# Kernel optimization log

Measured on AMD Instinct MI355X. Metric: run time of the kernel, lower is better.

The kernel has to match this reference:

```python
import jax, jax.numpy as jnp
import numpy as np

EMB = 128   # emb_dim
NT = 4      # n_ntype
ET = 38     # n_etype
H = 4       # head_count
DH = EMB // H


def _bn(x, g, b):
    # BatchNorm1d in training mode: batch stats, biased variance, eps=1e-5
    m = x.mean(0)
    v = ((x - m) ** 2).mean(0)
    return (x - m) * jax.lax.rsqrt(v + 1e-5) * g + b


def setup_inputs() -> dict:
    key = jax.random.key(0)
    ks = jax.random.split(key, 32)
    N, E, d = 20000, 320000, EMB
    fe = ET + 1 + 2 * NT  # 47 = edge one-hot + head/tail one-hots
    s = 0.05
    inp = {
        "x": jax.random.normal(ks[0], (N, d), jnp.float32),
        "node_feature_extra": jax.random.normal(ks[1], (N, d), jnp.float32),
        "edge_index": jax.random.randint(ks[2], (2, E), 0, N),
        "edge_type": jax.random.randint(ks[3], (E,), 0, ET),
        "node_type": jax.random.randint(ks[4], (N,), 0, NT),
        # edge_encoder: Linear(47,d) + BN(d) + ReLU + Linear(d,d)
        "We1": jax.random.normal(ks[5], (fe, d), jnp.float32) * s,
        "be1": jax.random.normal(ks[6], (d,), jnp.float32) * s,
        "ge": 1.0 + jax.random.normal(ks[7], (d,), jnp.float32) * 0.1,
        "bbe": jax.random.normal(ks[8], (d,), jnp.float32) * 0.1,
        "We2": jax.random.normal(ks[9], (d, d), jnp.float32) * s,
        "be2": jax.random.normal(ks[10], (d,), jnp.float32) * s,
        # attention linears
        "Wk": jax.random.normal(ks[11], (3 * d, d), jnp.float32) * s,
        "bk": jax.random.normal(ks[12], (d,), jnp.float32) * s,
        "Wm": jax.random.normal(ks[13], (3 * d, d), jnp.float32) * s,
        "bm": jax.random.normal(ks[14], (d,), jnp.float32) * s,
        "Wq": jax.random.normal(ks[15], (2 * d, d), jnp.float32) * s,
        "bq": jax.random.normal(ks[16], (d,), jnp.float32) * s,
        # output mlp: Linear(d,d) + BN(d) + ReLU + Linear(d,d)
        "Wo1": jax.random.normal(ks[17], (d, d), jnp.float32) * s,
        "bo1": jax.random.normal(ks[18], (d,), jnp.float32) * s,
        "go": 1.0 + jax.random.normal(ks[19], (d,), jnp.float32) * 0.1,
        "bbo": jax.random.normal(ks[20], (d,), jnp.float32) * 0.1,
        "Wo2": jax.random.normal(ks[21], (d, d), jnp.float32) * s,
        "bo2": jax.random.normal(ks[22], (d,), jnp.float32) * s,
    }
    return inp


def reference(x, node_feature_extra, edge_index, edge_type, node_type,
              We1, be1, ge, bbe, We2, be2, Wk, bk, Wm, bm, Wq, bq,
              Wo1, bo1, go, bbo, Wo2, bo2):
    N, d = x.shape
    src0, dst0 = edge_index[0], edge_index[1]

    # edge features: one-hot edge type (+ self-loop type ET) || head/tail node-type one-hots
    ev = jax.nn.one_hot(edge_type, ET + 1, dtype=x.dtype)                  # [E, 39]
    self_ev = jnp.zeros((N, ET + 1), x.dtype).at[:, ET].set(1.0)           # [N, 39]
    nvec = jax.nn.one_hot(node_type, NT, dtype=x.dtype)                    # [N, 4]
    ht = jnp.concatenate([nvec[src0], nvec[dst0]], 1)                      # [E, 8]
    sht = jnp.concatenate([nvec, nvec], 1)                                 # [N, 8]
    feats = jnp.concatenate([jnp.concatenate([ev, ht], 1),
                             jnp.concatenate([self_ev, sht], 1)], 0)       # [E+N, 47]

    # edge_encoder MLP (BN over all E+N rows, training-mode stats)
    edge_attr = jax.nn.relu(_bn(feats @ We1 + be1, ge, bbe)) @ We2 + be2   # [E+N, d]

    loop = jnp.arange(N)
    src = jnp.concatenate([src0, loop])   # message source / softmax groups
    dst = jnp.concatenate([dst0, loop])   # aggregation target (x_i)

    X2 = jnp.concatenate([x, node_feature_extra], 1)                       # [N, 2d]
    xi = X2[dst]                                                           # [Et, 2d]
    xj = X2[src]                                                           # [Et, 2d]

    # split matmuls == Linear(concat([x, edge_attr]))
    k = (xi @ Wk[:2 * d] + edge_attr @ Wk[2 * d:] + bk).reshape(-1, H, DH)
    m = (xj @ Wm[:2 * d] + edge_attr @ Wm[2 * d:] + bm).reshape(-1, H, DH)
    q = ((xj @ Wq + bq) / np.sqrt(DH).astype(np.float32)).reshape(-1, H, DH)
    scores = (q * k).sum(-1)                                               # [Et, H]

    # scatter softmax over source node index
    smax = jax.lax.stop_gradient(jax.ops.segment_max(scores, src, num_segments=N))
    ex = jnp.exp(scores - smax[src])
    denom = jax.ops.segment_sum(ex, src, num_segments=N)
    alpha = ex / (denom[src] + 1e-16)

    # degree rescaling
    cnt = jax.ops.segment_sum(jnp.ones((src.shape[0],), x.dtype), src, num_segments=N)[src]
    alpha = alpha * cnt[:, None]

    out_msg = (m * alpha[:, :, None]).reshape(-1, d)
    aggr = jax.ops.segment_sum(out_msg, dst, num_segments=N)               # [N, d]

    # output MLP
    return jax.nn.relu(_bn(aggr @ Wo1 + bo1, go, bbo)) @ Wo2 + bo2
```

## Files before the change

kernel.cpp:

```cpp
#include <hip/hip_runtime.h>
#include <math.h>


#define ET_N 38
#define NCOMBO 624
#define NB_CNT 64
#define HALF_MAX 10240

__global__ __launch_bounds__(256) void count_kernel(
    const int* __restrict__ ei, const int* __restrict__ et,
    const int* __restrict__ nt, int* __restrict__ ce,
    unsigned* __restrict__ ph, unsigned* __restrict__ ps,
    unsigned* __restrict__ pd, int E, int Et, int N) {
  __shared__ unsigned lcnt[HALF_MAX];
  __shared__ unsigned lhist[NCOMBO];
  const int b = blockIdx.x;
  const int half = blockIdx.y & 1, which = blockIdx.y >> 1;
  const int H = (N + 1) >> 1;
  const int lo = half * H, hi = min(N, lo + H);
  const int span = hi - lo;
  const bool do_ce = (which == 0 && half == 0);
  for (int i = threadIdx.x; i < span; i += 256) lcnt[i] = 0;
  if (do_ce)
    for (int i = threadIdx.x; i < NCOMBO; i += 256) lhist[i] = 0;
  __syncthreads();
  const int chunk = (Et + NB_CNT - 1) / NB_CNT;
  const int e0 = b * chunk, e1 = min(Et, e0 + chunk);
  for (int e = e0 + threadIdx.x; e < e1; e += 256) {
    if (which == 0) {
      int s = (e < E) ? ei[e] : e - E;
      if (s >= lo && s < hi) atomicAdd(&lcnt[s - lo], 1u);
      if (do_ce) {
        int d = (e < E) ? ei[E + e] : e - E;
        int t = (e < E) ? et[e] : ET_N;
        int c = t * 16 + nt[s] * 4 + nt[d];
        ce[e] = c;
        atomicAdd(&lhist[c], 1u);
      }
    } else {
      int d = (e < E) ? ei[E + e] : e - E;
      if (d >= lo && d < hi) atomicAdd(&lcnt[d - lo], 1u);
    }
  }
  __syncthreads();
  unsigned* out = (which == 0) ? ps : pd;
  for (int i = threadIdx.x; i < span; i += 256)
    out[(size_t)b * N + lo + i] = lcnt[i];
  if (do_ce)
    for (int i = threadIdx.x; i < NCOMBO; i += 256)
      ph[(size_t)b * NCOMBO + i] = lhist[i];
}

__global__ __launch_bounds__(128) void histred_kernel(
    const unsigned* __restrict__ ph, int* __restrict__ hist) {
  int c = blockIdx.x * 128 + threadIdx.x;
  if (c >= NCOMBO) return;
  unsigned s = 0;
  for (int b = 0; b < NB_CNT; b++) s += ph[(size_t)b * NCOMBO + c];
  hist[c] = (int)s;
}

__global__ __launch_bounds__(256) void cntred_kernel(
    const unsigned* __restrict__ ps, const unsigned* __restrict__ pd,
    int* __restrict__ scnt, int* __restrict__ dcnt, int N) {
  int i = blockIdx.x * 256 + threadIdx.x;
  if (i >= 2 * N) return;
  const unsigned* src = (i < N) ? ps : pd;
  int n = (i < N) ? i : i - N;
  unsigned s = 0;
  for (int b = 0; b < NB_CNT; b++) s += src[(size_t)b * N + n];
  if (i < N) scnt[n] = (int)s;
  else       dcnt[n] = (int)s;
}

__global__ __launch_bounds__(1024) void scan_kernel(
    const int* __restrict__ dcnt, int* __restrict__ doff, int n) {
  __shared__ int s[1024];
  int tid = threadIdx.x;
  int ch = (n + 1023) >> 10;
  int base = tid * ch;
  int sum = 0;
  for (int i = 0; i < ch; i++) { int idx = base + i; if (idx < n) sum += dcnt[idx]; }
  s[tid] = sum; __syncthreads();
  for (int off = 1; off < 1024; off <<= 1) {
    int v = (tid >= off) ? s[tid - off] : 0;
    __syncthreads();
    s[tid] += v;
    __syncthreads();
  }
  int run = (tid > 0) ? s[tid - 1] : 0;
  for (int i = 0; i < ch; i++) {
    int idx = base + i;
    if (idx < n) { doff[idx] = run; run += dcnt[idx]; }
  }
  if (tid == 1023) doff[n] = s[1023];
}

__global__ __launch_bounds__(256) void bucket_kernel(
    const int* __restrict__ ei, const int* __restrict__ ce,
    const int* __restrict__ doff, int* __restrict__ dctr,
    int* __restrict__ ebuck, unsigned* __restrict__ sb, int E, int Et) {
  int e = blockIdx.x * 256 + threadIdx.x;
  if (e >= Et) return;
  int s, d;
  if (e < E) { s = ei[e]; d = ei[E + e]; }
  else       { s = d = e - E; }
  int c = ce[e];
  int pos = atomicAdd(&dctr[(size_t)d * 16], 1);
  int idx = doff[d] + pos;
  ebuck[idx] = e;
  sb[idx] = (unsigned)s | ((unsigned)c << 15);
}

__global__ __launch_bounds__(128) void bnstats1_kernel(
    const int* __restrict__ hist, const float* __restrict__ We1,
    const float* __restrict__ be1, const float* __restrict__ ge,
    const float* __restrict__ bbe, float* __restrict__ a1,
    float* __restrict__ b1, float invR) {
  int j = threadIdx.x;
  float s1 = 0.f, s2 = 0.f;
  for (int c = 0; c < NCOMBO; c++) {
    int w = hist[c];
    if (!w) continue;
    int t = c >> 4, a = (c >> 2) & 3, b = c & 3;
    float v = We1[t * 128 + j] + We1[(39 + a) * 128 + j] + We1[(43 + b) * 128 + j] + be1[j];
    float wf = (float)w;
    s1 += wf * v;
    s2 += wf * v * v;
  }
  float mean = s1 * invR;
  float var  = s2 * invR - mean * mean;
  float av = ge[j] * rsqrtf(var + 1e-5f);
  a1[j] = av;
  b1[j] = bbe[j] - mean * av;
}

__global__ __launch_bounds__(256) void htab_kernel(
    const float* __restrict__ We1, const float* __restrict__ be1,
    const float* __restrict__ a1, const float* __restrict__ b1,
    float* __restrict__ H) {
  int i = blockIdx.x * 256 + threadIdx.x;
  if (i >= NCOMBO * 128) return;
  int c = i >> 7, j = i & 127;
  int t = c >> 4, a = (c >> 2) & 3, b = c & 3;
  float v = We1[t * 128 + j] + We1[(39 + a) * 128 + j] + We1[(43 + b) * 128 + j] + be1[j];
  H[i] = fmaxf(0.f, v * a1[j] + b1[j]);
}

template <class ALoad>
static __device__ __forceinline__ void gemm_body(
    ALoad aload, const float* __restrict__ B, const float* __restrict__ bias,
    float* __restrict__ C, int M, int K, float scale, int row0) {
  __shared__ float As[16][68];
  __shared__ float Bs[16][128];
  const int tid = threadIdx.x;
  const int ty = tid >> 4, tx = tid & 15;
  float acc[4][8];
#pragma unroll
  for (int i = 0; i < 4; i++)
#pragma unroll
    for (int j = 0; j < 8; j++) acc[i][j] = 0.f;

  const int ar = tid >> 2;
  const int ak = (tid & 3) << 2;
  const int bk = tid >> 5;
  const int bc = (tid & 31) << 2;

  for (int k0 = 0; k0 < K; k0 += 16) {
    float4 av = make_float4(0.f, 0.f, 0.f, 0.f);
    int grow = row0 + ar;
    if (grow < M) av = aload(grow, k0 + ak);
    As[ak + 0][ar] = av.x;
    As[ak + 1][ar] = av.y;
    As[ak + 2][ar] = av.z;
    As[ak + 3][ar] = av.w;
    float4 b0 = *(const float4*)(B + (size_t)(k0 + bk) * 128 + bc);
    float4 b1 = *(const float4*)(B + (size_t)(k0 + bk + 8) * 128 + bc);
    *(float4*)&Bs[bk][bc] = b0;
    *(float4*)&Bs[bk + 8][bc] = b1;
    __syncthreads();
#pragma unroll
    for (int kk = 0; kk < 16; kk++) {
      float4 a4 = *(const float4*)&As[kk][ty << 2];
      float4 p0 = *(const float4*)&Bs[kk][tx << 2];
      float4 p1 = *(const float4*)&Bs[kk][64 + (tx << 2)];
      float a_[4] = {a4.x, a4.y, a4.z, a4.w};
      float b_[8] = {p0.x, p0.y, p0.z, p0.w, p1.x, p1.y, p1.z, p1.w};
#pragma unroll
      for (int i = 0; i < 4; i++)
#pragma unroll
        for (int j = 0; j < 8; j++) acc[i][j] = fmaf(a_[i], b_[j], acc[i][j]);
    }
    __syncthreads();
  }
#pragma unroll
  for (int i = 0; i < 4; i++) {
    int gr = row0 + (ty << 2) + i;
    if (gr >= M) continue;
    float out[8];
#pragma unroll
    for (int j = 0; j < 8; j++) {
      int col = (j < 4) ? (tx << 2) + j : 64 + (tx << 2) + (j - 4);
      float bv = bias ? bias[col] : 0.f;
      out[j] = (acc[i][j] + bv) * scale;
    }
    float4* cp0 = (float4*)(C + (size_t)gr * 128 + (tx << 2));
    float4* cp1 = (float4*)(C + (size_t)gr * 128 + 64 + (tx << 2));
    cp0[0] = make_float4(out[0], out[1], out[2], out[3]);
    cp1[0] = make_float4(out[4], out[5], out[6], out[7]);
  }
}

__global__ __launch_bounds__(256) void tab2_kernel(
    const float* __restrict__ Ttab,
    const float* __restrict__ WkE, const float* __restrict__ bk,
    const float* __restrict__ WmE, const float* __restrict__ bm,
    float* __restrict__ Tk, float* __restrict__ Tm) {
  const int row0 = blockIdx.x * 64;
  const float* B    = blockIdx.y ? WmE : WkE;
  const float* bias = blockIdx.y ? bm : bk;
  float*       C    = blockIdx.y ? Tm : Tk;
  auto aload = [&](int grow, int k) -> float4 {
    return *(const float4*)(Ttab + (size_t)grow * 128 + k);
  };
  gemm_body(aload, B, bias, C, NCOMBO, 128, 1.0f, row0);
}

__global__ __launch_bounds__(256) void node3_kernel(
    const float* __restrict__ x, const float* __restrict__ nfe,
    const float* __restrict__ Wk, const float* __restrict__ Wm,
    const float* __restrict__ Wq, const float* __restrict__ bq,
    float* __restrict__ K1n, float* __restrict__ M1n, float* __restrict__ Qn,
    int N) {
  const int row0 = blockIdx.x * 64;
  const float* B;
  const float* bias;
  float* C;
  float scale;
  if (blockIdx.y == 0)      { B = Wk; bias = nullptr; C = K1n; scale = 1.0f; }
  else if (blockIdx.y == 1) { B = Wm; bias = nullptr; C = M1n; scale = 1.0f; }
  else                      { B = Wq; bias = bq;      C = Qn;  scale = 0.17677669529663687f; }
  auto aload = [&](int grow, int k) -> float4 {
    const float* src = (k < 128) ? x : nfe;
    return *(const float4*)(src + (size_t)grow * 128 + (k & 127));
  };
  gemm_body(aload, B, bias, C, N, 256, scale, row0);
}

template <bool TRANS>
__global__ __launch_bounds__(256) void gemm_plain(
    const float* __restrict__ A, const float* __restrict__ B,
    const float* __restrict__ bias, const float* __restrict__ ta,
    const float* __restrict__ tb, float* __restrict__ C,
    int M, int K, float scale) {
  const int row0 = blockIdx.x * 64;
  auto aload = [&](int grow, int k) -> float4 {
    float4 v = *(const float4*)(A + (size_t)grow * K + k);
    if (TRANS) {
      v.x = fmaxf(0.f, fmaf(v.x, ta[k + 0], tb[k + 0]));
      v.y = fmaxf(0.f, fmaf(v.y, ta[k + 1], tb[k + 1]));
      v.z = fmaxf(0.f, fmaf(v.z, ta[k + 2], tb[k + 2]));
      v.w = fmaxf(0.f, fmaf(v.w, ta[k + 3], tb[k + 3]));
    }
    return v;
  };
  gemm_body(aload, B, bias, C, M, K, scale, row0);
}

__global__ __launch_bounds__(256) void score_kernel(
    const int* __restrict__ ei, const int* __restrict__ ce,
    const float* __restrict__ Qn, const float* __restrict__ K1n,
    const float* __restrict__ Tk, float* __restrict__ ex,
    float* __restrict__ denomp, int E, int Et) {
  int g0 = (blockIdx.x * 8 + (threadIdx.x >> 5)) * 2;
  int lane = threadIdx.x & 31;
  if (g0 >= Et) return;
  int g1 = g0 + 1;
  bool v1 = g1 < Et;

  int s0, d0;
  if (g0 < E) { s0 = ei[g0]; d0 = ei[E + g0]; }
  else        { s0 = d0 = g0 - E; }
  int c0 = ce[g0];
  int s1 = 0, d1 = 0, c1 = 0;
  if (v1) {
    if (g1 < E) { s1 = ei[g1]; d1 = ei[E + g1]; }
    else        { s1 = d1 = g1 - E; }
    c1 = ce[g1];
  }

  float4 q0 = ((const float4*)(Qn  + (size_t)s0 * 128))[lane];
  float4 k0 = ((const float4*)(K1n + (size_t)d0 * 128))[lane];
  float4 t0 = ((const float4*)(Tk  + (size_t)c0 * 128))[lane];
  float4 q1 = ((const float4*)(Qn  + (size_t)s1 * 128))[lane];
  float4 k1 = ((const float4*)(K1n + (size_t)d1 * 128))[lane];
  float4 t1 = ((const float4*)(Tk  + (size_t)c1 * 128))[lane];

  float p0 = q0.x * (k0.x + t0.x) + q0.y * (k0.y + t0.y) +
             q0.z * (k0.z + t0.z) + q0.w * (k0.w + t0.w);
  float p1 = q1.x * (k1.x + t1.x) + q1.y * (k1.y + t1.y) +
             q1.z * (k1.z + t1.z) + q1.w * (k1.w + t1.w);
  p0 += __shfl_xor(p0, 4); p1 += __shfl_xor(p1, 4);
  p0 += __shfl_xor(p0, 2); p1 += __shfl_xor(p1, 2);
  p0 += __shfl_xor(p0, 1); p1 += __shfl_xor(p1, 1);

  if ((lane & 7) == 0) {
    int h = lane >> 3;
    float e0 = expf(p0);
    ex[(size_t)g0 * 4 + h] = e0;
    atomicAdd(&denomp[(size_t)s0 * 16 + h], e0);
    if (v1) {
      float e1 = expf(p1);
      ex[(size_t)g1 * 4 + h] = e1;
      atomicAdd(&denomp[(size_t)s1 * 16 + h], e1);
    }
  }
}

__global__ __launch_bounds__(256) void rden_kernel(
    const int* __restrict__ scnt, float* __restrict__ denomp, int N) {
  int i = blockIdx.x * 256 + threadIdx.x;
  if (i >= N * 4) return;
  int n = i >> 2, h = i & 3;
  float v = denomp[(size_t)n * 16 + h];
  denomp[(size_t)n * 16 + h] = (float)scnt[n] / (v + 1e-16f);
}

__global__ __launch_bounds__(256) void alphab_kernel(
    const int* __restrict__ ebuck, const unsigned* __restrict__ sb,
    const float* __restrict__ ex, const float* __restrict__ denomp,
    float* __restrict__ ab, int Et) {
  int idx = blockIdx.x * 256 + threadIdx.x;
  if (idx >= Et) return;
  int e = ebuck[idx];
  int s = sb[idx] & 0x7FFF;
  float4 exv = ((const float4*)ex)[e];
  float4 dn  = *(const float4*)&denomp[(size_t)s * 16];
  ((float4*)ab)[idx] = make_float4(exv.x * dn.x, exv.y * dn.y,
                                   exv.z * dn.z, exv.w * dn.w);
}

__global__ __launch_bounds__(256) void aggr_kernel(
    const unsigned* __restrict__ sb, const float* __restrict__ ab,
    const int* __restrict__ doff, const float* __restrict__ M1n,
    const float* __restrict__ Tm, float* __restrict__ aggr) {
  __shared__ float sacc[128];
  int n = blockIdx.x;
  int j = threadIdx.x & 127;
  int half = threadIdx.x >> 7;
  int h = j >> 5;
  float acc = 0.f;
  int i0 = doff[n], i1 = doff[n + 1];
  for (int base = i0 + half * 2; base < i1; base += 4) {
    int kA = base, kB = base + 1;
    unsigned pA = sb[kA];
    int sA = pA & 0x7FFF, cA = pA >> 15;
    float alA = ab[(size_t)kA * 4 + h];
    float mA = M1n[(size_t)sA * 128 + j] + Tm[(size_t)cA * 128 + j];
    bool vB = kB < i1;
    unsigned pB = vB ? sb[kB] : 0u;
    int sB = pB & 0x7FFF, cB = pB >> 15;
    float alB = vB ? ab[(size_t)kB * 4 + h] : 0.f;
    float mB = vB ? (M1n[(size_t)sB * 128 + j] + Tm[(size_t)cB * 128 + j]) : 0.f;
    acc += mA * alA;
    acc += mB * alB;
  }
  if (half == 1) sacc[j] = acc;
  __syncthreads();
  if (half == 0) aggr[(size_t)n * 128 + j] = acc + sacc[j];
}

__global__ __launch_bounds__(256) void colsum_kernel(
    const float* __restrict__ z, float* __restrict__ s1,
    float* __restrict__ s2, int M) {
  __shared__ float l1[256], l2[256];
  int j = threadIdx.x & 127;
  int half = threadIdx.x >> 7;
  float a = 0.f, b = 0.f;
  for (int r = blockIdx.x * 2 + half; r < M; r += gridDim.x * 2) {
    float v = z[(size_t)r * 128 + j];
    a += v;
    b += v * v;
  }
  l1[threadIdx.x] = a;
  l2[threadIdx.x] = b;
  __syncthreads();
  if (half == 0) {
    a = l1[j] + l1[j + 128];
    b = l2[j] + l2[j + 128];
    atomicAdd(&s1[j], a);
    atomicAdd(&s2[j], b);
  }
}

__global__ __launch_bounds__(128) void bnparam_kernel(
    const float* __restrict__ s1, const float* __restrict__ s2,
    const float* __restrict__ g, const float* __restrict__ bb,
    float* __restrict__ ta, float* __restrict__ tb, float invM) {
  int j = threadIdx.x;
  float mean = s1[j] * invM;
  float var = s2[j] * invM - mean * mean;
  float a = g[j] * rsqrtf(var + 1e-5f);
  ta[j] = a;
  tb[j] = bb[j] - mean * a;
}

extern "C" void kernel_launch(void* const* d_in, const int* in_sizes, int n_in,
                              void* d_out, int out_size, void* d_ws, size_t ws_size,
                              hipStream_t stream) {
  const float* x   = (const float*)d_in[0];
  const float* nfe = (const float*)d_in[1];
  const int*   ei  = (const int*)d_in[2];
  const int*   et  = (const int*)d_in[3];
  const int*   nt  = (const int*)d_in[4];
  const float* We1 = (const float*)d_in[5];
  const float* be1 = (const float*)d_in[6];
  const float* ge  = (const float*)d_in[7];
  const float* bbe = (const float*)d_in[8];
  const float* We2 = (const float*)d_in[9];
  const float* be2 = (const float*)d_in[10];
  const float* Wk  = (const float*)d_in[11];
  const float* bkb = (const float*)d_in[12];
  const float* Wm  = (const float*)d_in[13];
  const float* bmb = (const float*)d_in[14];
  const float* Wq  = (const float*)d_in[15];
  const float* bqb = (const float*)d_in[16];
  const float* Wo1 = (const float*)d_in[17];
  const float* bo1 = (const float*)d_in[18];
  const float* go  = (const float*)d_in[19];
  const float* bbo = (const float*)d_in[20];
  const float* Wo2 = (const float*)d_in[21];
  const float* bo2 = (const float*)d_in[22];

  const int N  = in_sizes[0] / 128;
  const int E  = in_sizes[3];
  const int Et = E + N;

  char* p = (char*)d_ws;
  auto alloc = [&](size_t bytes) -> char* {
    char* r = p;
    p += (bytes + 255) & ~(size_t)255;
    return r;
  };
  char* zero_base = p;
  int*   dctr  = (int*)alloc((size_t)N * 16 * 4);
  float* denomp= (float*)alloc((size_t)N * 16 * 4);
  float* cs1   = (float*)alloc(128 * 4);
  float* cs2   = (float*)alloc(128 * 4);
  size_t zero_bytes = (size_t)(p - zero_base);
  int*      ce   = (int*)alloc((size_t)Et * 4);
  int*      ebuck= (int*)alloc((size_t)Et * 4);
  unsigned* sb   = (unsigned*)alloc((size_t)Et * 4);
  int*      doff = (int*)alloc((size_t)(N + 1) * 4);
  int*      hist = (int*)alloc(NCOMBO * 4);
  int*      scnt = (int*)alloc((size_t)N * 4);
  int*      dcnt = (int*)alloc((size_t)N * 4);
  unsigned* ps   = (unsigned*)alloc((size_t)NB_CNT * N * 4);
  unsigned* pd   = (unsigned*)alloc((size_t)NB_CNT * N * 4);
  unsigned* ph   = (unsigned*)alloc((size_t)NB_CNT * NCOMBO * 4);
  float* a1    = (float*)alloc(128 * 4);
  float* b1    = (float*)alloc(128 * 4);
  float* a2    = (float*)alloc(128 * 4);
  float* b2    = (float*)alloc(128 * 4);
  float* Htab  = (float*)alloc((size_t)NCOMBO * 128 * 4);
  float* Ttab  = (float*)alloc((size_t)NCOMBO * 128 * 4);
  float* Tk    = (float*)alloc((size_t)NCOMBO * 128 * 4);
  float* Tm    = (float*)alloc((size_t)NCOMBO * 128 * 4);
  float* K1n   = (float*)alloc((size_t)N * 128 * 4);
  float* M1n   = (float*)alloc((size_t)N * 128 * 4);
  float* Qn    = (float*)alloc((size_t)N * 128 * 4);
  float* exbuf = (float*)alloc((size_t)Et * 4 * 4);
  float* ab    = (float*)alloc((size_t)Et * 4 * 4);
  float* aggr  = (float*)alloc((size_t)N * 128 * 4);
  float* z     = (float*)alloc((size_t)N * 128 * 4);
  (void)ws_size;

  hipMemsetAsync(zero_base, 0, zero_bytes, stream);

  count_kernel<<<dim3(NB_CNT, 4), 256, 0, stream>>>(ei, et, nt, ce, ph, ps, pd, E, Et, N);
  histred_kernel<<<(NCOMBO + 127) / 128, 128, 0, stream>>>(ph, hist);
  cntred_kernel<<<(2 * N + 255) / 256, 256, 0, stream>>>(ps, pd, scnt, dcnt, N);
  scan_kernel<<<1, 1024, 0, stream>>>(dcnt, doff, N);
  bucket_kernel<<<(Et + 255) / 256, 256, 0, stream>>>(ei, ce, doff, dctr, ebuck, sb, E, Et);
  bnstats1_kernel<<<1, 128, 0, stream>>>(hist, We1, be1, ge, bbe, a1, b1, 1.0f / (float)Et);
  htab_kernel<<<(NCOMBO * 128 + 255) / 256, 256, 0, stream>>>(We1, be1, a1, b1, Htab);
  gemm_plain<false><<<(NCOMBO + 63) / 64, 256, 0, stream>>>(Htab, We2, be2, nullptr, nullptr, Ttab, NCOMBO, 128, 1.0f);
  tab2_kernel<<<dim3((NCOMBO + 63) / 64, 2), 256, 0, stream>>>(Ttab, Wk + 256 * 128, bkb, Wm + 256 * 128, bmb, Tk, Tm);
  int gm = (N + 63) / 64;
  node3_kernel<<<dim3(gm, 3), 256, 0, stream>>>(x, nfe, Wk, Wm, Wq, bqb, K1n, M1n, Qn, N);
  score_kernel<<<(Et + 15) / 16, 256, 0, stream>>>(ei, ce, Qn, K1n, Tk, exbuf, denomp, E, Et);
  rden_kernel<<<(N * 4 + 255) / 256, 256, 0, stream>>>(scnt, denomp, N);
  alphab_kernel<<<(Et + 255) / 256, 256, 0, stream>>>(ebuck, sb, exbuf, denomp, ab, Et);
  aggr_kernel<<<N, 256, 0, stream>>>(sb, ab, doff, M1n, Tm, aggr);
  gemm_plain<false><<<gm, 256, 0, stream>>>(aggr, Wo1, bo1, nullptr, nullptr, z, N, 128, 1.0f);
  colsum_kernel<<<256, 256, 0, stream>>>(z, cs1, cs2, N);
  bnparam_kernel<<<1, 128, 0, stream>>>(cs1, cs2, go, bbo, a2, b2, 1.0f / (float)N);
  gemm_plain<true><<<gm, 256, 0, stream>>>(z, Wo2, bo2, a2, b2, (float*)d_out, N, 128, 1.0f);
}
```

Baseline: 527.4 us.

## Scatter exp scores into dst-bucket order and fold alpha into aggregation

The bucket kernel now records each edge's bucket position, so the score kernel writes exp values directly in destination-sorted order. This removes the alphab pass and its intermediate buffer; the aggregation kernel multiplies by the per-source reciprocal denominator inline and is unrolled four deep. The edge-encoder BN statistics are also split into a precomputed value table, a 16-block partial reduction and a separate parameter kernel. The BN+ReLU is applied inside the GEMM's A-load instead of through a separate htab pass. The cost is scattered 4-byte writes in the score kernel and an extra gather of denomp per edge in aggregation.

```diff
diff --git a/kernel.cpp b/kernel.cpp
--- a/kernel.cpp
+++ b/kernel.cpp
@@ -5,6 +5,7 @@
 #define ET_N 38
 #define NCOMBO 624
 #define NB_CNT 64
+#define NB_ST 16
 #define HALF_MAX 10240
 
 __global__ __launch_bounds__(256) void count_kernel(
@@ -99,7 +100,7 @@
 __global__ __launch_bounds__(256) void bucket_kernel(
     const int* __restrict__ ei, const int* __restrict__ ce,
     const int* __restrict__ doff, int* __restrict__ dctr,
-    int* __restrict__ ebuck, unsigned* __restrict__ sb, int E, int Et) {
+    unsigned* __restrict__ sb, int* __restrict__ ibuck, int E, int Et) {
   int e = blockIdx.x * 256 + threadIdx.x;
   if (e >= Et) return;
   int s, d;
@@ -108,43 +109,45 @@
   int c = ce[e];
   int pos = atomicAdd(&dctr[(size_t)d * 16], 1);
   int idx = doff[d] + pos;
-  ebuck[idx] = e;
   sb[idx] = (unsigned)s | ((unsigned)c << 15);
-}
-
-__global__ __launch_bounds__(128) void bnstats1_kernel(
-    const int* __restrict__ hist, const float* __restrict__ We1,
-    const float* __restrict__ be1, const float* __restrict__ ge,
-    const float* __restrict__ bbe, float* __restrict__ a1,
-    float* __restrict__ b1, float invR) {
+  ibuck[e] = idx;
+}
+
+__global__ __launch_bounds__(128) void vtab_kernel(
+    const float* __restrict__ We1, const float* __restrict__ be1,
+    float* __restrict__ vtab) {
+  int c = blockIdx.x, j = threadIdx.x;
+  int t = c >> 4, a = (c >> 2) & 3, b = c & 3;
+  vtab[(size_t)c * 128 + j] =
+      We1[t * 128 + j] + We1[(39 + a) * 128 + j] + We1[(43 + b) * 128 + j] + be1[j];
+}
+
+__global__ __launch_bounds__(128) void wstat_kernel(
+    const int* __restrict__ hist, const float* __restrict__ vtab,
+    float* __restrict__ bs1, float* __restrict__ bs2) {
   int j = threadIdx.x;
+  int b = blockIdx.x;
   float s1 = 0.f, s2 = 0.f;
-  for (int c = 0; c < NCOMBO; c++) {
-    int w = hist[c];
-    if (!w) continue;
-    int t = c >> 4, a = (c >> 2) & 3, b = c & 3;
-    float v = We1[t * 128 + j] + We1[(39 + a) * 128 + j] + We1[(43 + b) * 128 + j] + be1[j];
-    float wf = (float)w;
-    s1 += wf * v;
-    s2 += wf * v * v;
-  }
-  float mean = s1 * invR;
-  float var  = s2 * invR - mean * mean;
+  for (int c = b; c < NCOMBO; c += NB_ST) {
+    float w = (float)hist[c];
+    float v = vtab[(size_t)c * 128 + j];
+    s1 += w * v;
+    s2 += w * v * v;
+  }
+  atomicAdd(&bs1[j], s1);
+  atomicAdd(&bs2[j], s2);
+}
+
+__global__ __launch_bounds__(128) void bnp1_kernel(
+    const float* __restrict__ bs1, const float* __restrict__ bs2,
+    const float* __restrict__ ge, const float* __restrict__ bbe,
+    float* __restrict__ a1, float* __restrict__ b1, float invR) {
+  int j = threadIdx.x;
+  float mean = bs1[j] * invR;
+  float var  = bs2[j] * invR - mean * mean;
   float av = ge[j] * rsqrtf(var + 1e-5f);
   a1[j] = av;
   b1[j] = bbe[j] - mean * av;
-}
-
-__global__ __launch_bounds__(256) void htab_kernel(
-    const float* __restrict__ We1, const float* __restrict__ be1,
-    const float* __restrict__ a1, const float* __restrict__ b1,
-    float* __restrict__ H) {
-  int i = blockIdx.x * 256 + threadIdx.x;
-  if (i >= NCOMBO * 128) return;
-  int c = i >> 7, j = i & 127;
-  int t = c >> 4, a = (c >> 2) & 3, b = c & 3;
-  float v = We1[t * 128 + j] + We1[(39 + a) * 128 + j] + We1[(43 + b) * 128 + j] + be1[j];
-  H[i] = fmaxf(0.f, v * a1[j] + b1[j]);
 }
 
 template <class ALoad>
@@ -269,9 +272,9 @@
 
 __global__ __launch_bounds__(256) void score_kernel(
     const int* __restrict__ ei, const int* __restrict__ ce,
-    const float* __restrict__ Qn, const float* __restrict__ K1n,
-    const float* __restrict__ Tk, float* __restrict__ ex,
-    float* __restrict__ denomp, int E, int Et) {
+    const int* __restrict__ ibuck, const float* __restrict__ Qn,
+    const float* __restrict__ K1n, const float* __restrict__ Tk,
+    float* __restrict__ exb, float* __restrict__ denomp, int E, int Et) {
   int g0 = (blockIdx.x * 8 + (threadIdx.x >> 5)) * 2;
   int lane = threadIdx.x & 31;
   if (g0 >= Et) return;
@@ -306,12 +309,14 @@
 
   if ((lane & 7) == 0) {
     int h = lane >> 3;
+    int i0b = ibuck[g0];
     float e0 = expf(p0);
-    ex[(size_t)g0 * 4 + h] = e0;
+    exb[(size_t)i0b * 4 + h] = e0;
     atomicAdd(&denomp[(size_t)s0 * 16 + h], e0);
     if (v1) {
+      int i1b = ibuck[g1];
       float e1 = expf(p1);
-      ex[(size_t)g1 * 4 + h] = e1;
+      exb[(size_t)i1b * 4 + h] = e1;
       atomicAdd(&denomp[(size_t)s1 * 16 + h], e1);
     }
   }
@@ -326,24 +331,11 @@
   denomp[(size_t)n * 16 + h] = (float)scnt[n] / (v + 1e-16f);
 }
 
-__global__ __launch_bounds__(256) void alphab_kernel(
-    const int* __restrict__ ebuck, const unsigned* __restrict__ sb,
-    const float* __restrict__ ex, const float* __restrict__ denomp,
-    float* __restrict__ ab, int Et) {
-  int idx = blockIdx.x * 256 + threadIdx.x;
-  if (idx >= Et) return;
-  int e = ebuck[idx];
-  int s = sb[idx] & 0x7FFF;
-  float4 exv = ((const float4*)ex)[e];
-  float4 dn  = *(const float4*)&denomp[(size_t)s * 16];
-  ((float4*)ab)[idx] = make_float4(exv.x * dn.x, exv.y * dn.y,
-                                   exv.z * dn.z, exv.w * dn.w);
-}
-
 __global__ __launch_bounds__(256) void aggr_kernel(
-    const unsigned* __restrict__ sb, const float* __restrict__ ab,
-    const int* __restrict__ doff, const float* __restrict__ M1n,
-    const float* __restrict__ Tm, float* __restrict__ aggr) {
+    const unsigned* __restrict__ sb, const float* __restrict__ exb,
+    const float* __restrict__ denomp, const int* __restrict__ doff,
+    const float* __restrict__ M1n, const float* __restrict__ Tm,
+    float* __restrict__ aggr) {
   __shared__ float sacc[128];
   int n = blockIdx.x;
   int j = threadIdx.x & 127;
@@ -351,19 +343,17 @@
   int h = j >> 5;
   float acc = 0.f;
   int i0 = doff[n], i1 = doff[n + 1];
-  for (int base = i0 + half * 2; base < i1; base += 4) {
-    int kA = base, kB = base + 1;
-    unsigned pA = sb[kA];
-    int sA = pA & 0x7FFF, cA = pA >> 15;
-    float alA = ab[(size_t)kA * 4 + h];
-    float mA = M1n[(size_t)sA * 128 + j] + Tm[(size_t)cA * 128 + j];
-    bool vB = kB < i1;
-    unsigned pB = vB ? sb[kB] : 0u;
-    int sB = pB & 0x7FFF, cB = pB >> 15;
-    float alB = vB ? ab[(size_t)kB * 4 + h] : 0.f;
-    float mB = vB ? (M1n[(size_t)sB * 128 + j] + Tm[(size_t)cB * 128 + j]) : 0.f;
-    acc += mA * alA;
-    acc += mB * alB;
+  for (int base = i0 + half * 4; base < i1; base += 8) {
+#pragma unroll
+    for (int u = 0; u < 4; u++) {
+      int k = base + u;
+      if (k < i1) {
+        unsigned pk = sb[k];
+        int sk = pk & 0x7FFF, ck = pk >> 15;
+        float al = exb[(size_t)k * 4 + h] * denomp[(size_t)sk * 16 + h];
+        acc += (M1n[(size_t)sk * 128 + j] + Tm[(size_t)ck * 128 + j]) * al;
+      }
+    }
   }
   if (half == 1) sacc[j] = acc;
   __syncthreads();
@@ -447,10 +437,12 @@
   float* denomp= (float*)alloc((size_t)N * 16 * 4);
   float* cs1   = (float*)alloc(128 * 4);
   float* cs2   = (float*)alloc(128 * 4);
+  float* bs1   = (float*)alloc(128 * 4);
+  float* bs2   = (float*)alloc(128 * 4);
   size_t zero_bytes = (size_t)(p - zero_base);
   int*      ce   = (int*)alloc((size_t)Et * 4);
-  int*      ebuck= (int*)alloc((size_t)Et * 4);
   unsigned* sb   = (unsigned*)alloc((size_t)Et * 4);
+  int*      ibuck= (int*)alloc((size_t)Et * 4);
   int*      doff = (int*)alloc((size_t)(N + 1) * 4);
   int*      hist = (int*)alloc(NCOMBO * 4);
   int*      scnt = (int*)alloc((size_t)N * 4);
@@ -462,36 +454,35 @@
   float* b1    = (float*)alloc(128 * 4);
   float* a2    = (float*)alloc(128 * 4);
   float* b2    = (float*)alloc(128 * 4);
-  float* Htab  = (float*)alloc((size_t)NCOMBO * 128 * 4);
+  float* vtab  = (float*)alloc((size_t)NCOMBO * 128 * 4);
   float* Ttab  = (float*)alloc((size_t)NCOMBO * 128 * 4);
   float* Tk    = (float*)alloc((size_t)NCOMBO * 128 * 4);
   float* Tm    = (float*)alloc((size_t)NCOMBO * 128 * 4);
   float* K1n   = (float*)alloc((size_t)N * 128 * 4);
   float* M1n   = (float*)alloc((size_t)N * 128 * 4);
   float* Qn    = (float*)alloc((size_t)N * 128 * 4);
-  float* exbuf = (float*)alloc((size_t)Et * 4 * 4);
-  float* ab    = (float*)alloc((size_t)Et * 4 * 4);
+  float* exb   = (float*)alloc((size_t)Et * 4 * 4);
   float* aggr  = (float*)alloc((size_t)N * 128 * 4);
   float* z     = (float*)alloc((size_t)N * 128 * 4);
   (void)ws_size;
 
   hipMemsetAsync(zero_base, 0, zero_bytes, stream);
 
+  vtab_kernel<<<NCOMBO, 128, 0, stream>>>(We1, be1, vtab);
   count_kernel<<<dim3(NB_CNT, 4), 256, 0, stream>>>(ei, et, nt, ce, ph, ps, pd, E, Et, N);
   histred_kernel<<<(NCOMBO + 127) / 128, 128, 0, stream>>>(ph, hist);
   cntred_kernel<<<(2 * N + 255) / 256, 256, 0, stream>>>(ps, pd, scnt, dcnt, N);
   scan_kernel<<<1, 1024, 0, stream>>>(dcnt, doff, N);
-  bucket_kernel<<<(Et + 255) / 256, 256, 0, stream>>>(ei, ce, doff, dctr, ebuck, sb, E, Et);
-  bnstats1_kernel<<<1, 128, 0, stream>>>(hist, We1, be1, ge, bbe, a1, b1, 1.0f / (float)Et);
-  htab_kernel<<<(NCOMBO * 128 + 255) / 256, 256, 0, stream>>>(We1, be1, a1, b1, Htab);
-  gemm_plain<false><<<(NCOMBO + 63) / 64, 256, 0, stream>>>(Htab, We2, be2, nullptr, nullptr, Ttab, NCOMBO, 128, 1.0f);
+  bucket_kernel<<<(Et + 255) / 256, 256, 0, stream>>>(ei, ce, doff, dctr, sb, ibuck, E, Et);
+  wstat_kernel<<<NB_ST, 128, 0, stream>>>(hist, vtab, bs1, bs2);
+  bnp1_kernel<<<1, 128, 0, stream>>>(bs1, bs2, ge, bbe, a1, b1, 1.0f / (float)Et);
+  gemm_plain<true><<<(NCOMBO + 63) / 64, 256, 0, stream>>>(vtab, We2, be2, a1, b1, Ttab, NCOMBO, 128, 1.0f);
   tab2_kernel<<<dim3((NCOMBO + 63) / 64, 2), 256, 0, stream>>>(Ttab, Wk + 256 * 128, bkb, Wm + 256 * 128, bmb, Tk, Tm);
   int gm = (N + 63) / 64;
   node3_kernel<<<dim3(gm, 3), 256, 0, stream>>>(x, nfe, Wk, Wm, Wq, bqb, K1n, M1n, Qn, N);
-  score_kernel<<<(Et + 15) / 16, 256, 0, stream>>>(ei, ce, Qn, K1n, Tk, exbuf, denomp, E, Et);
+  score_kernel<<<(Et + 15) / 16, 256, 0, stream>>>(ei, ce, ibuck, Qn, K1n, Tk, exb, denomp, E, Et);
   rden_kernel<<<(N * 4 + 255) / 256, 256, 0, stream>>>(scnt, denomp, N);
-  alphab_kernel<<<(Et + 255) / 256, 256, 0, stream>>>(ebuck, sb, exbuf, denomp, ab, Et);
-  aggr_kernel<<<N, 256, 0, stream>>>(sb, ab, doff, M1n, Tm, aggr);
+  aggr_kernel<<<N, 256, 0, stream>>>(sb, exb, denomp, doff, M1n, Tm, aggr);
   gemm_plain<false><<<gm, 256, 0, stream>>>(aggr, Wo1, bo1, nullptr, nullptr, z, N, 128, 1.0f);
   colsum_kernel<<<256, 256, 0, stream>>>(z, cs1, cs2, N);
   bnparam_kernel<<<1, 128, 0, stream>>>(cs1, cs2, go, bbo, a2, b2, 1.0f / (float)N);
```

After: 466.1 us. 1.13x faster.
